# Performance work log

Measured on AMD Instinct MI355X. Metric: run time of the kernel, lower is better.

The kernel has to match this reference:

```python
import jax, jax.numpy as jnp
import numpy as np

WL = 8          # windowlen
LOSS_TH = 10.0  # losss threshold
BIT = 8


def _round(x):
    return jnp.round(x)


def part_quant1(x, mx, bitwidth, en=1):
    if en == 1:
        lsb = 2.0 ** (_round(jnp.log2(mx / 2.0 ** (bitwidth - 1))) + 1.0)
    else:
        lsb = 2.0 ** (_round(jnp.log2(mx / 2.0 ** bitwidth)) + 1.0)
    return _round(x / lsb) * lsb


def setup_inputs() -> dict:
    key = jax.random.key(0)
    x = jax.random.normal(key, (1, 16, 1024, 1024), dtype=jnp.float32)
    return {"x": x}


def reference(x):
    B, N, H, W = x.shape  # B must be 1
    wl = WL
    Wb, Hb = W // wl, H // wl

    # delta_comp: column-wise delta with zero pad on the left
    x_left = jnp.pad(x[..., : W - 1], ((0, 0), (0, 0), (0, 0), (1, 0)))
    xc = x - x_left

    In_max = jnp.abs(xc).max()
    x1 = part_quant1(xc, In_max, BIT, en=1)

    # blockify: d has shape (Wb, Hb, wl*wl, N); d1 is (Wb, Hb, N, wl*wl)
    b = x1.reshape(B, N, H, Wb, wl).transpose(0, 1, 3, 2, 4)           # B,N,Wb,H,wl
    c = b.reshape(B, N, Wb, Hb, wl, wl).transpose(0, 2, 3, 1, 4, 5)    # B,Wb,Hb,N,wl,wl
    d = c.reshape(B, Wb, Hb, N, wl * wl).transpose(0, 1, 2, 4, 3)[0]   # Wb,Hb,wl^2,N
    d1 = jnp.swapaxes(d, -1, -2)                                       # Wb,Hb,N,wl^2

    a1 = d1[:, :, 0:1, :]
    a2 = d1[:, :, 1:2, :]
    a3 = jnp.ones_like(a1)
    a_base = jnp.concatenate([a1, a2, a3], axis=2)                     # Wb,Hb,3,wl^2

    # blocks where both basis images are (near) constant
    flat = ((a1.max(-1) - a1.min(-1)).squeeze(-1) < 1e-6) & \
           ((a2.max(-1) - a2.min(-1)).squeeze(-1) < 1e-6)              # Wb,Hb

    ATA = jnp.einsum('whik,whjk->whij', a_base, a_base)                # Wb,Hb,3,3
    det = jnp.linalg.det(ATA)
    eye3 = jnp.eye(3, dtype=x.dtype)
    ATA = jnp.where((det == 0)[..., None, None], eye3, ATA)
    ATA_inv = jnp.linalg.inv(ATA)

    base = ATA_inv @ a_base                                            # Wb,Hb,3,wl^2
    p = base @ d                                                       # Wb,Hb,3,N
    r = jnp.swapaxes(a_base, -1, -2) @ p                               # Wb,Hb,wl^2,N
    r1 = part_quant1(jnp.swapaxes(r, -1, -2), In_max, BIT, en=1)       # Wb,Hb,N,wl^2

    loss_sum = ((d1 - r1) ** 2).sum(-1)                                # Wb,Hb,N
    rr = jnp.where((loss_sum <= LOSS_TH)[..., None], r1, d1)
    rr = jnp.where(flat[:, :, None, None], d1, rr)

    # deblockify back to (1, N, H, W)
    rr = rr.reshape(Wb, Hb, N, wl, wl).transpose(2, 1, 3, 0, 4).reshape(N, H, W)[None]

    # delta_dcom
    return rr + x_left
```

## Files before the change

### kernel.cpp

```cpp
#include <hip/hip_runtime.h>

static constexpr int Hh  = 1024;
static constexpr int Wd  = 1024;
static constexpr int NCH = 16;

__global__ __launch_bounds__(256) void k_maxabs(const float* __restrict__ x,
                                                unsigned int* __restrict__ omax,
                                                int n4) {
    float m = 0.0f;
    const int stride = gridDim.x * blockDim.x;
    const int lane = threadIdx.x & 63;
    for (int i = blockIdx.x * blockDim.x + threadIdx.x; i < n4; i += stride) {
        float4 v = reinterpret_cast<const float4*>(x)[i];
        float prevw = __shfl_up(v.w, 1);
        int w0 = (i * 4) & (Wd - 1);
        float left;
        if (w0 == 0) {
            left = 0.0f;
        } else if (lane == 0) {
            left = x[i * 4 - 1];
        } else {
            left = prevw;
        }
        float d0 = v.x - left;
        float d1 = v.y - v.x;
        float d2 = v.z - v.y;
        float d3 = v.w - v.z;
        m = fmaxf(m, fmaxf(fmaxf(fabsf(d0), fabsf(d1)), fmaxf(fabsf(d2), fabsf(d3))));
    }
#pragma unroll
    for (int off = 32; off >= 1; off >>= 1)
        m = fmaxf(m, __shfl_xor(m, off));
    __shared__ float smax[4];
    int wv = threadIdx.x >> 6;
    if (lane == 0) smax[wv] = m;
    __syncthreads();
    if (threadIdx.x == 0) {
        float mm = fmaxf(fmaxf(smax[0], smax[1]), fmaxf(smax[2], smax[3]));
        atomicMax(omax, __float_as_uint(mm));
    }
}

__device__ __forceinline__ float quantv(float v, float inv_lsb, float lsb) {
    return rintf(v * inv_lsb) * lsb;
}

__global__ __launch_bounds__(256) void k_blocks(const float* __restrict__ x,
                                                const unsigned int* __restrict__ pmax,
                                                float* __restrict__ out) {
    const int bid = blockIdx.x;
    const int xcd = bid & 7;
    const int lin = xcd * 256 + (bid >> 3);
    const int hb  = lin >> 4;
    const int wg  = lin & 15;
    const int w_base = wg * 64;
    const int h0     = hb * 8;
    const int tid = threadIdx.x;

    __shared__ float lds[68][129];

    for (int v = tid; v < 2048; v += 256) {
        const int row = v >> 4;
        const int j   = v & 15;
        const int ch  = row >> 3, r = row & 7;
        const int gidx = (ch * Hh + (h0 + r)) * Wd + w_base + j * 4;
        float4 val = *reinterpret_cast<const float4*>(x + gidx);
        lds[4 + j * 4 + 0][row] = val.x;
        lds[4 + j * 4 + 1][row] = val.y;
        lds[4 + j * 4 + 2][row] = val.z;
        lds[4 + j * 4 + 3][row] = val.w;
    }
    if (tid < 128) {
        const int row = tid;
        const int ch = row >> 3, r = row & 7;
        float4 val;
        if (wg == 0) {
            val = make_float4(0.f, 0.f, 0.f, 0.f);
        } else {
            const int gidx = (ch * Hh + (h0 + r)) * Wd + w_base - 4;
            val = *reinterpret_cast<const float4*>(x + gidx);
        }
        lds[0][row] = val.x;
        lds[1][row] = val.y;
        lds[2][row] = val.z;
        lds[3][row] = val.w;
    }
    __syncthreads();

    const float mx      = __uint_as_float(*pmax);
    const float lsb     = exp2f(rintf(log2f(mx * 0.0078125f)) + 1.0f);
    const float inv_lsb = 1.0f / lsb;

    const int ch = tid >> 4;
    const int g  = tid & 15;
    const int ri = g >> 1;
    const int jb = (g & 1) * 4;

    const int rowN = ch * 8 + ri;
    const int r0   = ri;
    const int r1   = 8 + ri;

    for (int sb = 0; sb < 8; ++sb) {
        const int cb = 4 + sb * 8 + jb;

        float xl[4], dvv[4], a1v[4], a2v[4];
#pragma unroll
        for (int q = 0; q < 4; ++q) {
            const int c = cb + q;
            xl[q]  = lds[c - 1][rowN];
            dvv[q] = quantv(lds[c][rowN] - xl[q], inv_lsb, lsb);
            a1v[q] = quantv(lds[c][r0] - lds[c - 1][r0], inv_lsb, lsb);
            a2v[q] = quantv(lds[c][r1] - lds[c - 1][r1], inv_lsb, lsb);
        }

        float s11 = 0.f, s12 = 0.f, s22 = 0.f, s1 = 0.f, s2 = 0.f;
        float mn1 = a1v[0], mx1 = a1v[0], mn2 = a2v[0], mx2 = a2v[0];
#pragma unroll
        for (int q = 0; q < 4; ++q) {
            s11 += a1v[q] * a1v[q];
            s12 += a1v[q] * a2v[q];
            s22 += a2v[q] * a2v[q];
            s1  += a1v[q];
            s2  += a2v[q];
            mn1 = fminf(mn1, a1v[q]); mx1 = fmaxf(mx1, a1v[q]);
            mn2 = fminf(mn2, a2v[q]); mx2 = fmaxf(mx2, a2v[q]);
        }
#pragma unroll
        for (int off = 1; off < 16; off <<= 1) {
            s11 += __shfl_xor(s11, off);
            s12 += __shfl_xor(s12, off);
            s22 += __shfl_xor(s22, off);
            s1  += __shfl_xor(s1,  off);
            s2  += __shfl_xor(s2,  off);
            mn1 = fminf(mn1, __shfl_xor(mn1, off));
            mx1 = fmaxf(mx1, __shfl_xor(mx1, off));
            mn2 = fminf(mn2, __shfl_xor(mn2, off));
            mx2 = fmaxf(mx2, __shfl_xor(mx2, off));
        }
        const bool flat = ((mx1 - mn1) < 1e-6f) && ((mx2 - mn2) < 1e-6f);

        const float a00 = s11, a01 = s12, a02 = s1;
        const float a10 = s12, a11 = s22, a12 = s2;
        const float a20 = s1,  a21 = s2,  a22 = 64.0f;
        const float det = a00 * a11 * a22 + a01 * a12 * a20 + a02 * a10 * a21
                        - a02 * a11 * a20 - a00 * a12 * a21 - a01 * a10 * a22;

        float i00, i01, i02, i11, i12, i22;
        if (det == 0.0f) {
            i00 = 1.f; i01 = 0.f; i02 = 0.f; i11 = 1.f; i12 = 0.f; i22 = 1.f;
        } else {
            const float rd = 1.0f / det;
            i00 = (a11 * a22 - a12 * a21) * rd;
            i01 = (a02 * a21 - a01 * a22) * rd;
            i02 = (a01 * a12 - a02 * a11) * rd;
            i11 = (a00 * a22 - a02 * a20) * rd;
            i12 = (a02 * a10 - a00 * a12) * rd;
            i22 = (a00 * a11 - a01 * a10) * rd;
        }

        float m0 = 0.f, m1 = 0.f, m2 = 0.f;
#pragma unroll
        for (int q = 0; q < 4; ++q) {
            m0 += a1v[q] * dvv[q];
            m1 += a2v[q] * dvv[q];
            m2 += dvv[q];
        }
#pragma unroll
        for (int off = 1; off < 16; off <<= 1) {
            m0 += __shfl_xor(m0, off);
            m1 += __shfl_xor(m1, off);
            m2 += __shfl_xor(m2, off);
        }
        const float p0 = i00 * m0 + i01 * m1 + i02 * m2;
        const float p1 = i01 * m0 + i11 * m1 + i12 * m2;
        const float p2 = i02 * m0 + i12 * m1 + i22 * m2;

        float r1v[4];
        float loss = 0.f;
#pragma unroll
        for (int q = 0; q < 4; ++q) {
            float r  = a1v[q] * p0 + a2v[q] * p1 + p2;
            r1v[q]   = quantv(r, inv_lsb, lsb);
            float df = dvv[q] - r1v[q];
            loss += df * df;
        }
#pragma unroll
        for (int off = 1; off < 16; off <<= 1)
            loss += __shfl_xor(loss, off);

        const bool use_r = (!flat) && (loss <= 10.0f);

        float4 o;
        o.x = (use_r ? r1v[0] : dvv[0]) + xl[0];
        o.y = (use_r ? r1v[1] : dvv[1]) + xl[1];
        o.z = (use_r ? r1v[2] : dvv[2]) + xl[2];
        o.w = (use_r ? r1v[3] : dvv[3]) + xl[3];

        const int oidx = (ch * Hh + (h0 + ri)) * Wd + w_base + sb * 8 + jb;
        *reinterpret_cast<float4*>(out + oidx) = o;
    }
}

extern "C" void kernel_launch(void* const* d_in, const int* in_sizes, int n_in,
                              void* d_out, int out_size, void* d_ws, size_t ws_size,
                              hipStream_t stream) {
    const float* x = (const float*)d_in[0];
    float* out     = (float*)d_out;
    unsigned int* pmax = (unsigned int*)d_ws;

    hipMemsetAsync(d_ws, 0, sizeof(unsigned int), stream);

    const int n4 = (NCH * Hh * Wd) / 4;
    k_maxabs<<<2048, 256, 0, stream>>>(x, pmax, n4);

    k_blocks<<<128 * 16, 256, 0, stream>>>(x, pmax, out);
}
```

Before: 172.3 us.

## Replace LDS staging in block kernel with direct global loads and lane shuffles

The block kernel no longer stages a 68x129 tile in shared memory behind a barrier. Each thread now loads its own row plus the two basis rows (channels 0 and 1) straight from global memory as float4, and takes the left neighbour from the adjacent lane via shuffle, carrying it across sub-blocks. Launch bounds are raised to ask for 8 blocks per SM. Removing LDS use and the barrier should allow more occupancy, at the cost of redundant global reads of the basis rows by every channel's threads, which are expected to hit in cache.

```diff
diff --git a/kernel.cpp b/kernel.cpp
--- a/kernel.cpp
+++ b/kernel.cpp
@@ -45,9 +45,9 @@
     return rintf(v * inv_lsb) * lsb;
 }
 
-__global__ __launch_bounds__(256) void k_blocks(const float* __restrict__ x,
-                                                const unsigned int* __restrict__ pmax,
-                                                float* __restrict__ out) {
+__global__ __launch_bounds__(256, 8) void k_blocks(const float* __restrict__ x,
+                                                   const unsigned int* __restrict__ pmax,
+                                                   float* __restrict__ out) {
     const int bid = blockIdx.x;
     const int xcd = bid & 7;
     const int lin = xcd * 256 + (bid >> 3);
@@ -57,61 +57,55 @@
     const int h0     = hb * 8;
     const int tid = threadIdx.x;
 
-    __shared__ float lds[68][129];
-
-    for (int v = tid; v < 2048; v += 256) {
-        const int row = v >> 4;
-        const int j   = v & 15;
-        const int ch  = row >> 3, r = row & 7;
-        const int gidx = (ch * Hh + (h0 + r)) * Wd + w_base + j * 4;
-        float4 val = *reinterpret_cast<const float4*>(x + gidx);
-        lds[4 + j * 4 + 0][row] = val.x;
-        lds[4 + j * 4 + 1][row] = val.y;
-        lds[4 + j * 4 + 2][row] = val.z;
-        lds[4 + j * 4 + 3][row] = val.w;
-    }
-    if (tid < 128) {
-        const int row = tid;
-        const int ch = row >> 3, r = row & 7;
-        float4 val;
-        if (wg == 0) {
-            val = make_float4(0.f, 0.f, 0.f, 0.f);
-        } else {
-            const int gidx = (ch * Hh + (h0 + r)) * Wd + w_base - 4;
-            val = *reinterpret_cast<const float4*>(x + gidx);
-        }
-        lds[0][row] = val.x;
-        lds[1][row] = val.y;
-        lds[2][row] = val.z;
-        lds[3][row] = val.w;
-    }
-    __syncthreads();
-
-    const float mx      = __uint_as_float(*pmax);
-    const float lsb     = exp2f(rintf(log2f(mx * 0.0078125f)) + 1.0f);
-    const float inv_lsb = 1.0f / lsb;
-
     const int ch = tid >> 4;
     const int g  = tid & 15;
     const int ri = g >> 1;
     const int jb = (g & 1) * 4;
 
-    const int rowN = ch * 8 + ri;
-    const int r0   = ri;
-    const int r1   = 8 + ri;
+    const float mx      = __uint_as_float(*pmax);
+    const float lsb     = exp2f(rintf(log2f(mx * 0.0078125f)) + 1.0f);
+    const float inv_lsb = 1.0f / lsb;
+
+    const int rowOwn = (ch * Hh + (h0 + ri)) * Wd;
+    const int row0   = (h0 + ri) * Wd;
+    const int row1   = (Hh + h0 + ri) * Wd;
+
+    float lO = 0.f, l0 = 0.f, l1 = 0.f;
+    if (wg != 0 && jb == 0) {
+        lO = x[rowOwn + w_base - 1];
+        l0 = x[row0   + w_base - 1];
+        l1 = x[row1   + w_base - 1];
+    }
 
     for (int sb = 0; sb < 8; ++sb) {
-        const int cb = 4 + sb * 8 + jb;
-
-        float xl[4], dvv[4], a1v[4], a2v[4];
-#pragma unroll
-        for (int q = 0; q < 4; ++q) {
-            const int c = cb + q;
-            xl[q]  = lds[c - 1][rowN];
-            dvv[q] = quantv(lds[c][rowN] - xl[q], inv_lsb, lsb);
-            a1v[q] = quantv(lds[c][r0] - lds[c - 1][r0], inv_lsb, lsb);
-            a2v[q] = quantv(lds[c][r1] - lds[c - 1][r1], inv_lsb, lsb);
-        }
+        const int cbase = w_base + sb * 8 + jb;
+        const float4 vO = *reinterpret_cast<const float4*>(x + rowOwn + cbase);
+        const float4 v0 = *reinterpret_cast<const float4*>(x + row0   + cbase);
+        const float4 v1 = *reinterpret_cast<const float4*>(x + row1   + cbase);
+
+        const float tO = __shfl_xor(vO.w, 1);
+        const float t0 = __shfl_xor(v0.w, 1);
+        const float t1 = __shfl_xor(v1.w, 1);
+        const float leftO = (jb == 0) ? lO : tO;
+        const float left0 = (jb == 0) ? l0 : t0;
+        const float left1 = (jb == 0) ? l1 : t1;
+        lO = tO; l0 = t0; l1 = t1;
+
+        float xl[4] = {leftO, vO.x, vO.y, vO.z};
+
+        float dvv[4], a1v[4], a2v[4];
+        dvv[0] = quantv(vO.x - leftO, inv_lsb, lsb);
+        dvv[1] = quantv(vO.y - vO.x,  inv_lsb, lsb);
+        dvv[2] = quantv(vO.z - vO.y,  inv_lsb, lsb);
+        dvv[3] = quantv(vO.w - vO.z,  inv_lsb, lsb);
+        a1v[0] = quantv(v0.x - left0, inv_lsb, lsb);
+        a1v[1] = quantv(v0.y - v0.x,  inv_lsb, lsb);
+        a1v[2] = quantv(v0.z - v0.y,  inv_lsb, lsb);
+        a1v[3] = quantv(v0.w - v0.z,  inv_lsb, lsb);
+        a2v[0] = quantv(v1.x - left1, inv_lsb, lsb);
+        a2v[1] = quantv(v1.y - v1.x,  inv_lsb, lsb);
+        a2v[2] = quantv(v1.z - v1.y,  inv_lsb, lsb);
+        a2v[3] = quantv(v1.w - v1.z,  inv_lsb, lsb);
 
         float s11 = 0.f, s12 = 0.f, s22 = 0.f, s1 = 0.f, s2 = 0.f;
         float mn1 = a1v[0], mx1 = a1v[0], mn2 = a2v[0], mx2 = a2v[0];
@@ -196,7 +190,7 @@
         o.z = (use_r ? r1v[2] : dvv[2]) + xl[2];
         o.w = (use_r ? r1v[3] : dvv[3]) + xl[3];
 
-        const int oidx = (ch * Hh + (h0 + ri)) * Wd + w_base + sb * 8 + jb;
+        const int oidx = rowOwn + w_base + sb * 8 + jb;
         *reinterpret_cast<float4*>(out + oidx) = o;
     }
 }
```

New measurement: 181.3 us. 5.2% more time.
